# Kernel optimization log

Measured on AMD Instinct MI355X. Metric: run time of the kernel, lower is better.

The kernel has to match this reference:

```python
import jax, jax.numpy as jnp
import numpy as np

B, T, K, D_E, D_K, U = 16, 256, 128, 256, 256, 128


def setup_inputs() -> dict:
    key = jax.random.key(0)
    ks = jax.random.split(key, 6)
    knowledge_onehot = jax.random.uniform(ks[0], (B, K, D_K), dtype=jnp.float32)
    encoder_outputs = jax.random.normal(ks[1], (B, T, D_E), dtype=jnp.float32)
    W1 = jax.random.normal(ks[2], (D_E, U), dtype=jnp.float32) * (1.0 / np.sqrt(D_E))
    b1 = jnp.zeros((U,), dtype=jnp.float32)
    W2 = jax.random.normal(ks[3], (D_K, U), dtype=jnp.float32) * (1.0 / np.sqrt(D_K))
    b2 = jnp.zeros((U,), dtype=jnp.float32)
    V = jax.random.normal(ks[4], (U, 1), dtype=jnp.float32) * (1.0 / np.sqrt(U))
    bV = jnp.zeros((1,), dtype=jnp.float32)
    return {"knowledge_onehot": knowledge_onehot, "encoder_outputs": encoder_outputs,
            "W1": W1, "b1": b1, "W2": W2, "b2": b2, "V": V, "bV": bV}


def reference(knowledge_onehot, encoder_outputs, W1, b1, W2, b2, V, bV):
    # Vectorized over all T timesteps (original used a Python loop).
    e = (jnp.einsum('btd,du->btu', encoder_outputs, W1) + b1)[:, :, None, :]   # [B,T,1,U]
    k = (jnp.einsum('bkd,du->bku', knowledge_onehot, W2) + b2)[:, None, :, :]  # [B,1,K,U]
    score = jnp.einsum('btku,uo->btko', jnp.tanh(e + k), V) + bV               # [B,T,K,1]
    attn = jax.nn.softmax(score, axis=2)                                        # softmax over K
    # weighted sum of knowledge vectors over K -> [B,T,D_K]
    context = jnp.einsum('btko,bkd->btd', attn, knowledge_onehot)
    return context
```

## Files before the change

### kernel.cpp

```cpp
#include <hip/hip_runtime.h>

#define B_  16
#define T_  256
#define K_  128
#define DK_ 256
#define U_  128
#define TT_ 4

#define SCALE_ 2.8853900817779268f

__device__ float g_E2[B_ * T_ * U_];
__device__ float g_Km2[B_ * K_ * U_];

__global__ __launch_bounds__(256) void gemm_both(const float* __restrict__ enc,
                                                 const float* __restrict__ W1,
                                                 const float* __restrict__ b1,
                                                 const float* __restrict__ knw,
                                                 const float* __restrict__ W2,
                                                 const float* __restrict__ b2) {
    __shared__ float Xs[16][256];

    const int blk  = blockIdx.x;
    const bool isE = blk < 256;
    const float* __restrict__ X    = isE ? enc : knw;
    const float* __restrict__ W    = isE ? W1 : W2;
    const float* __restrict__ bias = isE ? b1 : b2;
    float* __restrict__ Y          = isE ? g_E2 : g_Km2;
    const int row0 = (isE ? blk : blk - 256) * 16;
    const int tid  = threadIdx.x;

#pragma unroll
    for (int j = 0; j < 4; j++) {
        const int i  = tid + j * 256;
        const int rr = i >> 6, cc = i & 63;
        *(float4*)&Xs[rr][cc * 4] =
            *(const float4*)&X[(row0 + rr) * 256 + cc * 4];
    }
    __syncthreads();

    const int uc = tid & 31;
    const int rp = (tid >> 5) * 2;
    float4 a0 = {0.f, 0.f, 0.f, 0.f};
    float4 a1 = {0.f, 0.f, 0.f, 0.f};

    for (int d = 0; d < 256; d += 4) {
        const float4 xa = *(const float4*)&Xs[rp][d];
        const float4 xb = *(const float4*)&Xs[rp + 1][d];
        const float* wp = &W[d * 128 + uc * 4];
        const float4 w0 = *(const float4*)(wp);
        const float4 w1 = *(const float4*)(wp + 128);
        const float4 w2 = *(const float4*)(wp + 256);
        const float4 w3 = *(const float4*)(wp + 384);
        a0.x = fmaf(xa.x, w0.x, a0.x); a0.y = fmaf(xa.x, w0.y, a0.y);
        a0.z = fmaf(xa.x, w0.z, a0.z); a0.w = fmaf(xa.x, w0.w, a0.w);
        a0.x = fmaf(xa.y, w1.x, a0.x); a0.y = fmaf(xa.y, w1.y, a0.y);
        a0.z = fmaf(xa.y, w1.z, a0.z); a0.w = fmaf(xa.y, w1.w, a0.w);
        a0.x = fmaf(xa.z, w2.x, a0.x); a0.y = fmaf(xa.z, w2.y, a0.y);
        a0.z = fmaf(xa.z, w2.z, a0.z); a0.w = fmaf(xa.z, w2.w, a0.w);
        a0.x = fmaf(xa.w, w3.x, a0.x); a0.y = fmaf(xa.w, w3.y, a0.y);
        a0.z = fmaf(xa.w, w3.z, a0.z); a0.w = fmaf(xa.w, w3.w, a0.w);
        a1.x = fmaf(xb.x, w0.x, a1.x); a1.y = fmaf(xb.x, w0.y, a1.y);
        a1.z = fmaf(xb.x, w0.z, a1.z); a1.w = fmaf(xb.x, w0.w, a1.w);
        a1.x = fmaf(xb.y, w1.x, a1.x); a1.y = fmaf(xb.y, w1.y, a1.y);
        a1.z = fmaf(xb.y, w1.z, a1.z); a1.w = fmaf(xb.y, w1.w, a1.w);
        a1.x = fmaf(xb.z, w2.x, a1.x); a1.y = fmaf(xb.z, w2.y, a1.y);
        a1.z = fmaf(xb.z, w2.z, a1.z); a1.w = fmaf(xb.z, w2.w, a1.w);
        a1.x = fmaf(xb.w, w3.x, a1.x); a1.y = fmaf(xb.w, w3.y, a1.y);
        a1.z = fmaf(xb.w, w3.z, a1.z); a1.w = fmaf(xb.w, w3.w, a1.w);
    }

    const float4 b4 = *(const float4*)&bias[uc * 4];
    float4 o0, o1;
    o0.x = __builtin_amdgcn_exp2f(SCALE_ * (a0.x + b4.x));
    o0.y = __builtin_amdgcn_exp2f(SCALE_ * (a0.y + b4.y));
    o0.z = __builtin_amdgcn_exp2f(SCALE_ * (a0.z + b4.z));
    o0.w = __builtin_amdgcn_exp2f(SCALE_ * (a0.w + b4.w));
    o1.x = __builtin_amdgcn_exp2f(SCALE_ * (a1.x + b4.x));
    o1.y = __builtin_amdgcn_exp2f(SCALE_ * (a1.y + b4.y));
    o1.z = __builtin_amdgcn_exp2f(SCALE_ * (a1.z + b4.z));
    o1.w = __builtin_amdgcn_exp2f(SCALE_ * (a1.w + b4.w));
    *(float4*)&Y[(row0 + rp) * 128 + uc * 4]     = o0;
    *(float4*)&Y[(row0 + rp + 1) * 128 + uc * 4] = o1;
}

__global__ __launch_bounds__(256, 4) void attn_ctx(const float* __restrict__ knw,
                                                   const float* __restrict__ V,
                                                   float* __restrict__ out) {
    __shared__ float sm[4][TT_][256];
    __shared__ float E2s[TT_][U_];
    __shared__ float attn[TT_][K_];

    float* const pA  = &sm[0][0][0];
    float* const V2s = &sm[1][0][0];

    const int tid  = threadIdx.x;
    const int blk  = blockIdx.x;
    const int b    = blk >> 6;
    const int t0   = (blk & 63) * TT_;
    const int lane = tid & 63;
    const int wave = tid >> 6;

    if (tid < 128) V2s[tid] = 2.0f * V[tid];
    if (tid < 128) {
        const int ti = tid >> 5, uc = tid & 31;
        *(float4*)&E2s[ti][uc * 4] =
            *(const float4*)&g_E2[(b * T_ + t0 + ti) * U_ + uc * 4];
    }

    const int k_idx = tid & 127;
    const int half  = tid >> 7;
    float4 km[16];
    {
        const float* kp = &g_Km2[(b * K_ + k_idx) * U_ + half * 64];
#pragma unroll
        for (int c = 0; c < 16; c++) km[c] = *(const float4*)&kp[c * 4];
    }
    __syncthreads();

    {
        float na[TT_] = {0.f, 0.f, 0.f, 0.f};
#pragma unroll
        for (int c = 0; c < 16; c++) {
            const float4 v4 = *(const float4*)&V2s[half * 64 + c * 4];
#pragma unroll
            for (int t = 0; t < TT_; t++) {
                const float4 e4 = *(const float4*)&E2s[t][half * 64 + c * 4];
                float r;
                r = __builtin_amdgcn_rcpf(fmaf(e4.x, km[c].x, 1.0f));
                na[t] = fmaf(v4.x, r, na[t]);
                r = __builtin_amdgcn_rcpf(fmaf(e4.y, km[c].y, 1.0f));
                na[t] = fmaf(v4.y, r, na[t]);
                r = __builtin_amdgcn_rcpf(fmaf(e4.z, km[c].z, 1.0f));
                na[t] = fmaf(v4.z, r, na[t]);
                r = __builtin_amdgcn_rcpf(fmaf(e4.w, km[c].w, 1.0f));
                na[t] = fmaf(v4.w, r, na[t]);
            }
        }
#pragma unroll
        for (int t = 0; t < TT_; t++) pA[t * 256 + tid] = na[t];
    }
    __syncthreads();

    {
        const int t = wave;
        const float* p = &pA[t * 256];
        float s0 = -(p[lane] + p[128 + lane]);
        float s1 = -(p[64 + lane] + p[192 + lane]);
        float m = fmaxf(s0, s1);
#pragma unroll
        for (int off = 32; off >= 1; off >>= 1)
            m = fmaxf(m, __shfl_xor(m, off));
        const float e0 = __builtin_amdgcn_exp2f(1.4426950408889634f * (s0 - m));
        const float e1 = __builtin_amdgcn_exp2f(1.4426950408889634f * (s1 - m));
        float ss = e0 + e1;
#pragma unroll
        for (int off = 32; off >= 1; off >>= 1)
            ss += __shfl_xor(ss, off);
        const float rinv = __builtin_amdgcn_rcpf(ss);
        attn[t][lane]      = e0 * rinv;
        attn[t][64 + lane] = e1 * rinv;
    }
    __syncthreads();

    {
        const int kg = wave, dq = lane;
        float4 acc[TT_];
#pragma unroll
        for (int ti = 0; ti < TT_; ti++) acc[ti] = make_float4(0.f, 0.f, 0.f, 0.f);

        const float* kp = &knw[(b * K_ + kg * 32) * DK_ + dq * 4];
#pragma unroll 4
        for (int ki = 0; ki < 32; ki++) {
            const float4 kn = *(const float4*)&kp[ki * DK_];
#pragma unroll
            for (int ti = 0; ti < TT_; ti++) {
                const float a = attn[ti][kg * 32 + ki];
                acc[ti].x = fmaf(a, kn.x, acc[ti].x);
                acc[ti].y = fmaf(a, kn.y, acc[ti].y);
                acc[ti].z = fmaf(a, kn.z, acc[ti].z);
                acc[ti].w = fmaf(a, kn.w, acc[ti].w);
            }
        }
#pragma unroll
        for (int ti = 0; ti < TT_; ti++)
            *(float4*)&sm[kg][ti][dq * 4] = acc[ti];
    }
    __syncthreads();

    {
        const int ti = tid >> 6, dd = tid & 63;
        const float4 s0 = *(const float4*)&sm[0][ti][dd * 4];
        const float4 s1 = *(const float4*)&sm[1][ti][dd * 4];
        const float4 s2 = *(const float4*)&sm[2][ti][dd * 4];
        const float4 s3 = *(const float4*)&sm[3][ti][dd * 4];
        float4 o;
        o.x = s0.x + s1.x + s2.x + s3.x;
        o.y = s0.y + s1.y + s2.y + s3.y;
        o.z = s0.z + s1.z + s2.z + s3.z;
        o.w = s0.w + s1.w + s2.w + s3.w;
        *(float4*)&out[(b * T_ + t0 + ti) * DK_ + dd * 4] = o;
    }
}

extern "C" void kernel_launch(void* const* d_in, const int* in_sizes, int n_in,
                              void* d_out, int out_size, void* d_ws,
                              size_t ws_size, hipStream_t stream) {
    (void)in_sizes; (void)n_in; (void)d_ws; (void)ws_size; (void)out_size;
    const float* knw = (const float*)d_in[0];
    const float* enc = (const float*)d_in[1];
    const float* W1  = (const float*)d_in[2];
    const float* b1  = (const float*)d_in[3];
    const float* W2  = (const float*)d_in[4];
    const float* b2  = (const float*)d_in[5];
    const float* V   = (const float*)d_in[6];
    float* out = (float*)d_out;

    gemm_both<<<384, 256, 0, stream>>>(enc, W1, b1, knw, W2, b2);
    attn_ctx<<<B_ * (T_ / TT_), 256, 0, stream>>>(knw, V, out);
}
```

Measured before the change: 104.4 us.

## Fuse encoder projection into attention kernel and split-K the knowledge GEMM

The encoder projection E = exp(2(enc·W1+b1)) is no longer computed in a separate GEMM and stored to global memory. Each attention block now computes its own 4 rows inside attn_ctx, with a split-K over 8 groups and a shared-memory reduction. The first kernel only handles the knowledge projection, using 128 blocks with a 4-way split-K and 8 rows per thread to raise register reuse. This removes the g_E2 global round trip and shrinks the first kernel. In exchange each attention block reads W1 (128KB) again from cache, adds an extra barrier, and uses more shared memory, which may lower occupancy.

```diff
diff --git a/kernel.cpp b/kernel.cpp
--- a/kernel.cpp
+++ b/kernel.cpp
@@ -9,89 +9,75 @@
 
 #define SCALE_ 2.8853900817779268f
 
-__device__ float g_E2[B_ * T_ * U_];
 __device__ float g_Km2[B_ * K_ * U_];
 
-__global__ __launch_bounds__(256) void gemm_both(const float* __restrict__ enc,
-                                                 const float* __restrict__ W1,
-                                                 const float* __restrict__ b1,
-                                                 const float* __restrict__ knw,
-                                                 const float* __restrict__ W2,
-                                                 const float* __restrict__ b2) {
+__global__ __launch_bounds__(256) void gemm_km(const float* __restrict__ knw,
+                                               const float* __restrict__ W2,
+                                               const float* __restrict__ b2) {
     __shared__ float Xs[16][256];
-
-    const int blk  = blockIdx.x;
-    const bool isE = blk < 256;
-    const float* __restrict__ X    = isE ? enc : knw;
-    const float* __restrict__ W    = isE ? W1 : W2;
-    const float* __restrict__ bias = isE ? b1 : b2;
-    float* __restrict__ Y          = isE ? g_E2 : g_Km2;
-    const int row0 = (isE ? blk : blk - 256) * 16;
+    __shared__ float part[4][16][128];
+
     const int tid  = threadIdx.x;
+    const int row0 = blockIdx.x * 16;
 
 #pragma unroll
     for (int j = 0; j < 4; j++) {
         const int i  = tid + j * 256;
         const int rr = i >> 6, cc = i & 63;
         *(float4*)&Xs[rr][cc * 4] =
-            *(const float4*)&X[(row0 + rr) * 256 + cc * 4];
-    }
-    __syncthreads();
-
-    const int uc = tid & 31;
-    const int rp = (tid >> 5) * 2;
-    float4 a0 = {0.f, 0.f, 0.f, 0.f};
-    float4 a1 = {0.f, 0.f, 0.f, 0.f};
-
-    for (int d = 0; d < 256; d += 4) {
-        const float4 xa = *(const float4*)&Xs[rp][d];
-        const float4 xb = *(const float4*)&Xs[rp + 1][d];
-        const float* wp = &W[d * 128 + uc * 4];
-        const float4 w0 = *(const float4*)(wp);
-        const float4 w1 = *(const float4*)(wp + 128);
-        const float4 w2 = *(const float4*)(wp + 256);
-        const float4 w3 = *(const float4*)(wp + 384);
-        a0.x = fmaf(xa.x, w0.x, a0.x); a0.y = fmaf(xa.x, w0.y, a0.y);
-        a0.z = fmaf(xa.x, w0.z, a0.z); a0.w = fmaf(xa.x, w0.w, a0.w);
-        a0.x = fmaf(xa.y, w1.x, a0.x); a0.y = fmaf(xa.y, w1.y, a0.y);
-        a0.z = fmaf(xa.y, w1.z, a0.z); a0.w = fmaf(xa.y, w1.w, a0.w);
-        a0.x = fmaf(xa.z, w2.x, a0.x); a0.y = fmaf(xa.z, w2.y, a0.y);
-        a0.z = fmaf(xa.z, w2.z, a0.z); a0.w = fmaf(xa.z, w2.w, a0.w);
-        a0.x = fmaf(xa.w, w3.x, a0.x); a0.y = fmaf(xa.w, w3.y, a0.y);
-        a0.z = fmaf(xa.w, w3.z, a0.z); a0.w = fmaf(xa.w, w3.w, a0.w);
-        a1.x = fmaf(xb.x, w0.x, a1.x); a1.y = fmaf(xb.x, w0.y, a1.y);
-        a1.z = fmaf(xb.x, w0.z, a1.z); a1.w = fmaf(xb.x, w0.w, a1.w);
-        a1.x = fmaf(xb.y, w1.x, a1.x); a1.y = fmaf(xb.y, w1.y, a1.y);
-        a1.z = fmaf(xb.y, w1.z, a1.z); a1.w = fmaf(xb.y, w1.w, a1.w);
-        a1.x = fmaf(xb.z, w2.x, a1.x); a1.y = fmaf(xb.z, w2.y, a1.y);
-        a1.z = fmaf(xb.z, w2.z, a1.z); a1.w = fmaf(xb.z, w2.w, a1.w);
-        a1.x = fmaf(xb.w, w3.x, a1.x); a1.y = fmaf(xb.w, w3.y, a1.y);
-        a1.z = fmaf(xb.w, w3.z, a1.z); a1.w = fmaf(xb.w, w3.w, a1.w);
-    }
-
-    const float4 b4 = *(const float4*)&bias[uc * 4];
-    float4 o0, o1;
-    o0.x = __builtin_amdgcn_exp2f(SCALE_ * (a0.x + b4.x));
-    o0.y = __builtin_amdgcn_exp2f(SCALE_ * (a0.y + b4.y));
-    o0.z = __builtin_amdgcn_exp2f(SCALE_ * (a0.z + b4.z));
-    o0.w = __builtin_amdgcn_exp2f(SCALE_ * (a0.w + b4.w));
-    o1.x = __builtin_amdgcn_exp2f(SCALE_ * (a1.x + b4.x));
-    o1.y = __builtin_amdgcn_exp2f(SCALE_ * (a1.y + b4.y));
-    o1.z = __builtin_amdgcn_exp2f(SCALE_ * (a1.z + b4.z));
-    o1.w = __builtin_amdgcn_exp2f(SCALE_ * (a1.w + b4.w));
-    *(float4*)&Y[(row0 + rp) * 128 + uc * 4]     = o0;
-    *(float4*)&Y[(row0 + rp + 1) * 128 + uc * 4] = o1;
+            *(const float4*)&knw[(row0 + rr) * 256 + cc * 4];
+    }
+    __syncthreads();
+
+    {
+        const int uc = tid & 31;
+        const int dq = (tid >> 5) & 3;
+        const int rh = tid >> 7;
+        float4 acc[8];
+#pragma unroll
+        for (int r = 0; r < 8; r++) acc[r] = make_float4(0.f, 0.f, 0.f, 0.f);
+#pragma unroll 8
+        for (int j = 0; j < 64; j++) {
+            const int d = dq * 64 + j;
+            const float4 w = *(const float4*)&W2[d * U_ + uc * 4];
+#pragma unroll
+            for (int r = 0; r < 8; r++) {
+                const float x = Xs[rh * 8 + r][d];
+                acc[r].x = fmaf(x, w.x, acc[r].x);
+                acc[r].y = fmaf(x, w.y, acc[r].y);
+                acc[r].z = fmaf(x, w.z, acc[r].z);
+                acc[r].w = fmaf(x, w.w, acc[r].w);
+            }
+        }
+#pragma unroll
+        for (int r = 0; r < 8; r++)
+            *(float4*)&part[dq][rh * 8 + r][uc * 4] = acc[r];
+    }
+    __syncthreads();
+
+#pragma unroll
+    for (int i = 0; i < 8; i++) {
+        const int idx = tid + i * 256;
+        const int r = idx >> 7, u = idx & 127;
+        float s = b2[u];
+#pragma unroll
+        for (int dq = 0; dq < 4; dq++) s += part[dq][r][u];
+        g_Km2[(row0 + r) * U_ + u] = __builtin_amdgcn_exp2f(SCALE_ * s);
+    }
 }
 
 __global__ __launch_bounds__(256, 4) void attn_ctx(const float* __restrict__ knw,
+                                                   const float* __restrict__ enc,
+                                                   const float* __restrict__ W1,
+                                                   const float* __restrict__ b1,
                                                    const float* __restrict__ V,
                                                    float* __restrict__ out) {
     __shared__ float sm[4][TT_][256];
+    __shared__ float encs[TT_][256];
     __shared__ float E2s[TT_][U_];
     __shared__ float attn[TT_][K_];
-
-    float* const pA  = &sm[0][0][0];
-    float* const V2s = &sm[1][0][0];
+    __shared__ float V2s[U_];
+    float* const smf = &sm[0][0][0];
 
     const int tid  = threadIdx.x;
     const int blk  = blockIdx.x;
@@ -100,12 +86,39 @@
     const int lane = tid & 63;
     const int wave = tid >> 6;
 
-    if (tid < 128) V2s[tid] = 2.0f * V[tid];
-    if (tid < 128) {
-        const int ti = tid >> 5, uc = tid & 31;
-        *(float4*)&E2s[ti][uc * 4] =
-            *(const float4*)&g_E2[(b * T_ + t0 + ti) * U_ + uc * 4];
-    }
+    {
+        const int rr = tid >> 6, cc = tid & 63;
+        *(float4*)&encs[rr][cc * 4] =
+            *(const float4*)&enc[(b * T_ + t0 + rr) * 256 + cc * 4];
+        if (tid < 128) V2s[tid] = 2.0f * V[tid];
+    }
+    __syncthreads();
+
+    {
+        const int uc = tid & 31;
+        const int dq = tid >> 5;
+        float4 a0 = {0,0,0,0}, a1 = {0,0,0,0}, a2 = {0,0,0,0}, a3 = {0,0,0,0};
+#pragma unroll 8
+        for (int j = 0; j < 32; j++) {
+            const int d = dq * 32 + j;
+            const float4 w = *(const float4*)&W1[d * U_ + uc * 4];
+            const float e0 = encs[0][d], e1 = encs[1][d];
+            const float e2 = encs[2][d], e3 = encs[3][d];
+            a0.x = fmaf(e0, w.x, a0.x); a0.y = fmaf(e0, w.y, a0.y);
+            a0.z = fmaf(e0, w.z, a0.z); a0.w = fmaf(e0, w.w, a0.w);
+            a1.x = fmaf(e1, w.x, a1.x); a1.y = fmaf(e1, w.y, a1.y);
+            a1.z = fmaf(e1, w.z, a1.z); a1.w = fmaf(e1, w.w, a1.w);
+            a2.x = fmaf(e2, w.x, a2.x); a2.y = fmaf(e2, w.y, a2.y);
+            a2.z = fmaf(e2, w.z, a2.z); a2.w = fmaf(e2, w.w, a2.w);
+            a3.x = fmaf(e3, w.x, a3.x); a3.y = fmaf(e3, w.y, a3.y);
+            a3.z = fmaf(e3, w.z, a3.z); a3.w = fmaf(e3, w.w, a3.w);
+        }
+        *(float4*)&smf[(dq * 4 + 0) * 128 + uc * 4] = a0;
+        *(float4*)&smf[(dq * 4 + 1) * 128 + uc * 4] = a1;
+        *(float4*)&smf[(dq * 4 + 2) * 128 + uc * 4] = a2;
+        *(float4*)&smf[(dq * 4 + 3) * 128 + uc * 4] = a3;
+    }
+    __syncthreads();
 
     const int k_idx = tid & 127;
     const int half  = tid >> 7;
@@ -115,7 +128,21 @@
 #pragma unroll
         for (int c = 0; c < 16; c++) km[c] = *(const float4*)&kp[c * 4];
     }
-    __syncthreads();
+
+    {
+        const int ti = tid >> 6, uu = tid & 63;
+#pragma unroll
+        for (int h = 0; h < 128; h += 64) {
+            float s = b1[uu + h];
+#pragma unroll
+            for (int dq = 0; dq < 8; dq++)
+                s += smf[(dq * 4 + ti) * 128 + uu + h];
+            E2s[ti][uu + h] = __builtin_amdgcn_exp2f(SCALE_ * s);
+        }
+    }
+    __syncthreads();
+
+    float* const pA = smf;
 
     {
         float na[TT_] = {0.f, 0.f, 0.f, 0.f};
@@ -183,16 +210,16 @@
         }
 #pragma unroll
         for (int ti = 0; ti < TT_; ti++)
-            *(float4*)&sm[kg][ti][dq * 4] = acc[ti];
+            *(float4*)&smf[(kg * TT_ + ti) * 256 + dq * 4] = acc[ti];
     }
     __syncthreads();
 
     {
         const int ti = tid >> 6, dd = tid & 63;
-        const float4 s0 = *(const float4*)&sm[0][ti][dd * 4];
-        const float4 s1 = *(const float4*)&sm[1][ti][dd * 4];
-        const float4 s2 = *(const float4*)&sm[2][ti][dd * 4];
-        const float4 s3 = *(const float4*)&sm[3][ti][dd * 4];
+        const float4 s0 = *(const float4*)&smf[(0 * TT_ + ti) * 256 + dd * 4];
+        const float4 s1 = *(const float4*)&smf[(1 * TT_ + ti) * 256 + dd * 4];
+        const float4 s2 = *(const float4*)&smf[(2 * TT_ + ti) * 256 + dd * 4];
+        const float4 s3 = *(const float4*)&smf[(3 * TT_ + ti) * 256 + dd * 4];
         float4 o;
         o.x = s0.x + s1.x + s2.x + s3.x;
         o.y = s0.y + s1.y + s2.y + s3.y;
@@ -215,6 +242,6 @@
     const float* V   = (const float*)d_in[6];
     float* out = (float*)d_out;
 
-    gemm_both<<<384, 256, 0, stream>>>(enc, W1, b1, knw, W2, b2);
-    attn_ctx<<<B_ * (T_ / TT_), 256, 0, stream>>>(knw, V, out);
+    gemm_km<<<128, 256, 0, stream>>>(knw, W2, b2);
+    attn_ctx<<<B_ * (T_ / TT_), 256, 0, stream>>>(knw, enc, W1, b1, V, out);
 }
```

Result: faster. 102.2 us (median of 2 runs) (-2.1%).
